# Kernel tuning notes

Measured on AMD Instinct MI355X. Metric: run time of the kernel, lower is better.

Reference implementation:

```python
import jax, jax.numpy as jnp
import numpy as np

N, E, NG = 4096, 8192, 256
AF, BF, H, L = 9, 4, 128, 3
LN_EPS = 1e-5


def _layernorm(x, g, b):
    mu = jnp.mean(x, axis=-1, keepdims=True)
    var = jnp.var(x, axis=-1, keepdims=True)
    return (x - mu) * jax.lax.rsqrt(var + LN_EPS) * g + b


def setup_inputs() -> dict:
    key = jax.random.key(0)
    ks = jax.random.split(key, 20)
    x = jax.random.normal(ks[0], (N, AF), dtype=jnp.float32)
    edge_index = jax.random.randint(ks[1], (2, E), 0, N, dtype=jnp.int64)
    edge_attr = jax.random.normal(ks[2], (E, BF), dtype=jnp.float32)
    batch = jnp.sort(jax.random.randint(ks[3], (N,), 0, NG, dtype=jnp.int64))
    s = lambda f: 1.0 / np.sqrt(f)
    return {
        "x": x, "edge_index": edge_index, "edge_attr": edge_attr, "batch": batch,
        "atom_w": jax.random.normal(ks[4], (AF, H), jnp.float32) * s(AF),
        "atom_b": jnp.zeros((H,), jnp.float32),
        # per-layer edge-network params, stacked over L layers
        "e1_w": jax.random.normal(ks[5], (L, BF, H), jnp.float32) * s(BF),
        "e1_b": jnp.zeros((L, H), jnp.float32),
        "e2_w": jax.random.normal(ks[6], (L, H, H * H), jnp.float32) * s(H),
        "e2_b": jnp.zeros((L, H * H), jnp.float32),
        "root_w": jax.random.normal(ks[7], (L, H, H), jnp.float32) * s(H),
        "conv_b": jnp.zeros((L, H), jnp.float32),
        "ln_g": jnp.ones((L, H), jnp.float32),
        "ln_b": jnp.zeros((L, H), jnp.float32),
        "head_w1": jax.random.normal(ks[8], (H, H // 2), jnp.float32) * s(H),
        "head_b1": jnp.zeros((H // 2,), jnp.float32),
        "head_w2": jax.random.normal(ks[9], (H // 2, 1), jnp.float32) * s(H // 2),
        "head_b2": jnp.zeros((1,), jnp.float32),
    }


def reference(x, edge_index, edge_attr, batch, atom_w, atom_b, e1_w, e1_b,
              e2_w, e2_b, root_w, conv_b, ln_g, ln_b, head_w1, head_b1,
              head_w2, head_b2):
    src, dst = edge_index[0], edge_index[1]
    h = jax.nn.relu(x @ atom_w + atom_b)  # [N, H]
    # in-degree for mean aggregation (empty -> 0 via clamp on denominator)
    deg = jax.ops.segment_sum(jnp.ones((E,), h.dtype), dst, num_segments=N)
    denom = jnp.maximum(deg, 1.0)[:, None]
    for l in range(L):
        # edge network: bond features -> per-edge HxH weight matrix
        eh = jax.nn.gelu(edge_attr @ e1_w[l] + e1_b[l], approximate=False)
        w = (eh @ e2_w[l] + e2_b[l]).reshape(E, H, H)  # [E, H, H]
        # gather source node features, per-edge matvec, scatter-mean to dst
        msg = jnp.einsum('ei,eio->eo', h[src], w)  # [E, H]
        agg = jax.ops.segment_sum(msg, dst, num_segments=N) / denom
        h_new = jax.nn.relu(agg + h @ root_w[l] + conv_b[l])
        h = _layernorm(h + h_new, ln_g[l], ln_b[l])
        # dropout: eval mode (identity)
    # global mean pool over graphs
    cnt = jnp.maximum(jax.ops.segment_sum(jnp.ones((N,), h.dtype), batch, num_segments=NG), 1.0)
    mol = jax.ops.segment_sum(h, batch, num_segments=NG) / cnt[:, None]
    hid = jax.nn.gelu(mol @ head_w1 + head_b1, approximate=False)
    logits = (hid @ head_w2 + head_b2).squeeze(-1)  # [NG]
    return logits
```

## Files before the change

kernel.cpp:

```cpp
#include <hip/hip_runtime.h>
#include <hip/hip_bf16.h>

#define N_NODES 4096
#define N_EDGES 8192
#define NGRAPH  256
#define AFEAT   9
#define BFEAT   4
#define H       128
#define NL      3
#define KS      129
#define SPLITS  4
#define TILE_E  64
#define NPB     4
#define SLICE_SH    16384
#define SLICE_BYTES 32768

typedef short short8 __attribute__((ext_vector_type(8)));
typedef float f32x4 __attribute__((ext_vector_type(4)));

__device__ __forceinline__ short f2b(float f){
    union { float f; unsigned u; } c; c.f = f;
    unsigned r = c.u + 0x7FFFu + ((c.u >> 16) & 1u);
    return (short)(r >> 16);
}
__device__ __forceinline__ float gelu_exact(float x){
    return 0.5f * x * (1.0f + erff(x * 0.70710678118654752440f));
}

__global__ void k_prep_b(const float* __restrict__ e2w, const float* __restrict__ e2b,
                         short* __restrict__ bt){
    __shared__ float ts[H][33];
    int b  = blockIdx.x;
    int o0 = (b & 3) * 32;
    int k  = (b >> 2) % KS;
    int l  = (b >> 2) / KS;
    const float* src = (k < H) ? (e2w + ((size_t)l * H + k) * (H * H))
                               : (e2b + (size_t)l * (H * H));
    for (int idx = threadIdx.x; idx < H * 32; idx += 256){
        int i = idx >> 5, op = idx & 31;
        ts[i][op] = src[i * H + o0 + op];
    }
    __syncthreads();
    short* dst = bt + (size_t)(l * KS + k) * SLICE_SH;
    for (int idx = threadIdx.x; idx < 32 * H; idx += 256){
        int j    = idx & 7;
        int quad = (idx >> 3) & 3;
        int op   = (idx >> 5) & 31;
        int ic   = idx >> 10;
        int i    = ic * 32 + quad * 8 + j;
        int o    = o0 + op;
        dst[((((o >> 4) * 4 + ic) * 64) + quad * 16 + (o & 15)) * 8 + j] = f2b(ts[i][op]);
    }
}

__global__ void k_atom(const float* __restrict__ x, const float* __restrict__ aw,
                       const float* __restrict__ ab, float* __restrict__ h,
                       short* __restrict__ hb){
    __shared__ float xs[AFEAT];
    int n = blockIdx.x, o = threadIdx.x;
    if (o < AFEAT) xs[o] = x[n * AFEAT + o];
    __syncthreads();
    float a = ab[o];
    #pragma unroll
    for (int f = 0; f < AFEAT; ++f) a += xs[f] * aw[f * H + o];
    a = fmaxf(a, 0.0f);
    h[(size_t)n * H + o]  = a;
    hb[(size_t)n * H + o] = f2b(a);
}

__global__ void k_deg(const int* __restrict__ ei, int* __restrict__ ideg){
    int e = blockIdx.x * 256 + threadIdx.x;
    if (e < N_EDGES) atomicAdd(&ideg[ei[N_EDGES + e]], 1);
}

__global__ void k_scan(const int* __restrict__ ideg, int* __restrict__ row_ptr,
                       int* __restrict__ cursor){
    __shared__ int part[256];
    int t = threadIdx.x;
    int base = t * 16;
    int loc[16]; int s = 0;
    #pragma unroll
    for (int i = 0; i < 16; ++i){ loc[i] = s; s += ideg[base + i]; }
    part[t] = s;
    __syncthreads();
    if (t == 0){
        int run = 0;
        for (int i = 0; i < 256; ++i){ int v = part[i]; part[i] = run; run += v; }
        row_ptr[N_NODES] = run;
    }
    __syncthreads();
    int off = part[t];
    #pragma unroll
    for (int i = 0; i < 16; ++i){
        row_ptr[base + i] = off + loc[i];
        cursor[base + i]  = off + loc[i];
    }
}

__global__ void k_fill(const int* __restrict__ ei, int* __restrict__ cursor,
                       int* __restrict__ eidx){
    int e = blockIdx.x * 256 + threadIdx.x;
    if (e < N_EDGES){
        int d = ei[N_EDGES + e];
        int pos = atomicAdd(&cursor[d], 1);
        eidx[pos] = e;
    }
}

__global__ void k_edge_mlp(const float* __restrict__ ea, const float* __restrict__ w1,
                           const float* __restrict__ b1, float* __restrict__ ehT){
    int o = blockIdx.x >> 5;
    int e = (blockIdx.x & 31) * 256 + threadIdx.x;
    float4 a = *(const float4*)(ea + (size_t)e * BFEAT);
    #pragma unroll
    for (int l = 0; l < NL; ++l){
        float v = b1[l * H + o]
                + a.x * w1[(l * BFEAT + 0) * H + o]
                + a.y * w1[(l * BFEAT + 1) * H + o]
                + a.z * w1[(l * BFEAT + 2) * H + o]
                + a.w * w1[(l * BFEAT + 3) * H + o];
        v = gelu_exact(v);
        ehT[((size_t)l * KS + o) * N_EDGES + e] = v;
        if (o == 0) ehT[((size_t)l * KS + H) * N_EDGES + e] = 1.0f;
    }
}

__global__ __launch_bounds__(256, 2)
void k_msg_gemm(const short* __restrict__ bt, const float* __restrict__ ehT,
                const short* __restrict__ hb, const int* __restrict__ ei,
                float* __restrict__ parts, int l){
    __shared__ __align__(16) float ehs[33 * TILE_E];

    const int tid  = threadIdx.x;
    const int lane = tid & 63, w = tid >> 6;
    const int col  = lane & 15, quad = lane >> 4;

    const int so    = blockIdx.x & 7;
    const int split = so & 3;
    const int ohalf = so >> 2;
    const int tile  = blockIdx.x >> 3;
    const int t     = ohalf * 4 + w;
    const int kbeg  = (KS * split) >> 2;
    const int kend  = (KS * (split + 1)) >> 2;
    const int kcnt  = kend - kbeg;
    const int ebase = tile * TILE_E;

    for (int idx = tid; idx < kcnt * TILE_E; idx += 256){
        int kk = idx >> 6, e = idx & 63;
        ehs[idx] = ehT[((size_t)(l * KS + kbeg + kk)) * N_EDGES + ebase + e];
    }

    short8 gf[4][4];
    #pragma unroll
    for (int m = 0; m < 4; ++m){
        int e = ebase + m * 16 + col;
        int s = ei[e];
        const char* gb = (const char*)hb + ((size_t)s * H + quad * 8) * 2;
        #pragma unroll
        for (int ic = 0; ic < 4; ++ic)
            gf[m][ic] = *(const short8*)(gb + ic * 64);
    }

    float acc[4][4];
    #pragma unroll
    for (int m = 0; m < 4; ++m)
        #pragma unroll
        for (int r = 0; r < 4; ++r) acc[m][r] = 0.0f;

    const char* bsrc = (const char*)bt + (size_t)(l * KS + kbeg) * SLICE_BYTES
                     + t * 4096 + lane * 16;

    short8 X[4], Y[4], Z[4];

    auto loadB = [&](short8 (&B)[4], int kk){
        const char* p = bsrc + (size_t)kk * SLICE_BYTES;
        #pragma unroll
        for (int ic = 0; ic < 4; ++ic)
            B[ic] = *(const short8*)(p + ic * 1024);
    };
    auto computeB = [&](const short8 (&B)[4], int kk){
        #pragma unroll
        for (int m = 0; m < 4; ++m){
            f32x4 ev = *(const f32x4*)(ehs + kk * TILE_E + m * 16 + quad * 4);
            f32x4 U = {0.0f, 0.0f, 0.0f, 0.0f};
            #pragma unroll
            for (int ic = 0; ic < 4; ++ic)
                U = __builtin_amdgcn_mfma_f32_16x16x32_bf16(gf[m][ic], B[ic], U, 0, 0, 0);
            #pragma unroll
            for (int r = 0; r < 4; ++r)
                acc[m][r] += ev[r] * U[r];
        }
    };

    loadB(X, 0); loadB(Y, 1); loadB(Z, 2);
    __syncthreads();

    int kk = 0;
    for (; kk + 3 < kcnt; kk += 3){
        computeB(X, kk);     loadB(X, kk + 3);
        computeB(Y, kk + 1); if (kk + 4 < kcnt) loadB(Y, kk + 4);
        computeB(Z, kk + 2); if (kk + 5 < kcnt) loadB(Z, kk + 5);
    }
    computeB(X, kk);
    if (kk + 1 < kcnt) computeB(Y, kk + 1);
    if (kk + 2 < kcnt) computeB(Z, kk + 2);

    float* pb = parts + (size_t)split * N_EDGES * H + (size_t)ebase * H + t * 16;
    #pragma unroll
    for (int m = 0; m < 4; ++m)
        #pragma unroll
        for (int r = 0; r < 4; ++r)
            pb[(size_t)(m * 16 + quad * 4 + r) * H + col] = acc[m][r];
}

__global__ void k_node(const float* __restrict__ parts, const int* __restrict__ eidx,
                       const int* __restrict__ row_ptr,
                       const float* __restrict__ rw, const float* __restrict__ cb,
                       const float* __restrict__ lg, const float* __restrict__ lb,
                       float* __restrict__ h, short* __restrict__ hb,
                       const int* __restrict__ batch, float* __restrict__ molsum,
                       float* __restrict__ cnt, int l, int dolast){
    __shared__ float hs[NPB][H];
    __shared__ float red[NPB][2][2];
    int n0 = blockIdx.x * NPB, o = threadIdx.x;
    const float* W = rw + (size_t)l * H * H;

    float hv[NPB], root[NPB], a[NPB];
    #pragma unroll
    for (int m = 0; m < NPB; ++m){
        hv[m] = h[(size_t)(n0 + m) * H + o];
        hs[m][o] = hv[m];
        root[m] = cb[l * H + o];
    }
    __syncthreads();

    #pragma unroll
    for (int m = 0; m < NPB; ++m){
        int p0 = row_ptr[n0 + m], p1 = row_ptr[n0 + m + 1];
        float s = 0.0f;
        for (int p = p0; p < p1; ++p){
            const float* pr = parts + (size_t)eidx[p] * H + o;
            #pragma unroll
            for (int sp = 0; sp < SPLITS; ++sp) s += pr[(size_t)sp * N_EDGES * H];
        }
        int d = p1 - p0;
        a[m] = s / (float)(d > 0 ? d : 1);
    }

    #pragma unroll 8
    for (int i = 0; i < H; ++i){
        float wv = W[i * H + o];
        #pragma unroll
        for (int m = 0; m < NPB; ++m) root[m] += hs[m][i] * wv;
    }

    float v[NPB];
    #pragma unroll
    for (int m = 0; m < NPB; ++m){
        float hn = fmaxf(a[m] + root[m], 0.0f);
        v[m] = hv[m] + hn;
        float s = v[m], q = v[m] * v[m];
        #pragma unroll
        for (int off = 32; off > 0; off >>= 1){
            s += __shfl_down(s, off, 64);
            q += __shfl_down(q, off, 64);
        }
        if ((o & 63) == 0){ red[m][0][o >> 6] = s; red[m][1][o >> 6] = q; }
    }
    __syncthreads();
    #pragma unroll
    for (int m = 0; m < NPB; ++m){
        float S = red[m][0][0] + red[m][0][1];
        float Q = red[m][1][0] + red[m][1][1];
        float mean = S * (1.0f / H);
        float var  = Q * (1.0f / H) - mean * mean;
        float out  = (v[m] - mean) * rsqrtf(var + 1e-5f) * lg[l * H + o] + lb[l * H + o];
        int n = n0 + m;
        h[(size_t)n * H + o]  = out;
        hb[(size_t)n * H + o] = f2b(out);
        if (dolast){
            int b = batch[n];
            atomicAdd(&molsum[b * H + o], out);
            if (o == 0) atomicAdd(&cnt[b], 1.0f);
        }
    }
}

__global__ void k_head(const float* __restrict__ molsum, const float* __restrict__ cnt,
                       const float* __restrict__ w1, const float* __restrict__ b1,
                       const float* __restrict__ w2, const float* __restrict__ b2,
                       float* __restrict__ out){
    __shared__ float mol[H];
    int g = blockIdx.x, t = threadIdx.x;
    float c = fmaxf(cnt[g], 1.0f);
    mol[t]      = molsum[g * H + t] / c;
    mol[t + 64] = molsum[g * H + t + 64] / c;
    __syncthreads();
    float a = b1[t];
    #pragma unroll 8
    for (int i = 0; i < H; ++i) a += mol[i] * w1[i * 64 + t];
    float hid = gelu_exact(a);
    float p = hid * w2[t];
    #pragma unroll
    for (int off = 32; off > 0; off >>= 1) p += __shfl_down(p, off, 64);
    if (t == 0) out[g] = p + b2[0];
}

extern "C" void kernel_launch(void* const* d_in, const int* in_sizes, int n_in,
                              void* d_out, int out_size, void* d_ws, size_t ws_size,
                              hipStream_t stream){
    (void)in_sizes; (void)n_in; (void)out_size; (void)ws_size;
    const float* x     = (const float*)d_in[0];
    const int*   ei    = (const int*)  d_in[1];
    const float* ea    = (const float*)d_in[2];
    const int*   batch = (const int*)  d_in[3];
    const float* aw    = (const float*)d_in[4];
    const float* ab    = (const float*)d_in[5];
    const float* e1w   = (const float*)d_in[6];
    const float* e1b   = (const float*)d_in[7];
    const float* e2w   = (const float*)d_in[8];
    const float* e2b   = (const float*)d_in[9];
    const float* rw    = (const float*)d_in[10];
    const float* cb    = (const float*)d_in[11];
    const float* lg    = (const float*)d_in[12];
    const float* lb    = (const float*)d_in[13];
    const float* hw1   = (const float*)d_in[14];
    const float* hb1   = (const float*)d_in[15];
    const float* hw2   = (const float*)d_in[16];
    const float* hb2   = (const float*)d_in[17];
    float* out = (float*)d_out;

    char* p = (char*)d_ws;
    auto carve = [&](size_t bytes){ char* r = p; p += (bytes + 255) & ~(size_t)255; return r; };
    short* bt     = (short*)carve((size_t)NL * KS * SLICE_SH * 2);
    float* h      = (float*)carve((size_t)N_NODES * H * 4);
    short* hbuf   = (short*)carve((size_t)N_NODES * H * 2);
    float* ehT    = (float*)carve((size_t)NL * KS * N_EDGES * 4);
    float* parts  = (float*)carve((size_t)SPLITS * N_EDGES * H * 4);
    int*   ideg   = (int*)  carve((size_t)N_NODES * 4);
    int*   row_ptr= (int*)  carve((size_t)(N_NODES + 1) * 4);
    int*   cursor = (int*)  carve((size_t)N_NODES * 4);
    int*   eidx   = (int*)  carve((size_t)N_EDGES * 4);
    float* molsum = (float*)carve((size_t)NGRAPH * H * 4);
    float* cnt    = (float*)carve((size_t)NGRAPH * 4);

    hipMemsetAsync(ideg, 0, (size_t)N_NODES * 4, stream);
    hipMemsetAsync(molsum, 0, (size_t)NGRAPH * H * 4, stream);
    hipMemsetAsync(cnt, 0, (size_t)NGRAPH * 4, stream);

    k_prep_b<<<NL * KS * 4, 256, 0, stream>>>(e2w, e2b, bt);
    k_atom<<<N_NODES, H, 0, stream>>>(x, aw, ab, h, hbuf);
    k_deg<<<N_EDGES / 256, 256, 0, stream>>>(ei, ideg);
    k_scan<<<1, 256, 0, stream>>>(ideg, row_ptr, cursor);
    k_fill<<<N_EDGES / 256, 256, 0, stream>>>(ei, cursor, eidx);
    k_edge_mlp<<<H * (N_EDGES / 256), 256, 0, stream>>>(ea, e1w, e1b, ehT);

    for (int l = 0; l < NL; ++l){
        k_msg_gemm<<<(N_EDGES / TILE_E) * 8, 256, 0, stream>>>(bt, ehT, hbuf, ei, parts, l);
        k_node<<<N_NODES / NPB, H, 0, stream>>>(parts, eidx, row_ptr, rw, cb, lg, lb,
                                                h, hbuf, batch, molsum, cnt, l,
                                                l == NL - 1 ? 1 : 0);
    }
    k_head<<<NGRAPH, 64, 0, stream>>>(molsum, cnt, hw1, hb1, hw2, hb2, out);
}
```

Baseline: 307.6 us.

## Switch message GEMM to 32x32x16 MFMA tiles with two-wave blocks

Rewrites the per-edge message GEMM to use the 32x32x16 bf16 MFMA instruction instead of 16x16x32. The pre-packed edge-weight layout, the source-feature gather, the accumulator shape and the output store are all reorganised to match the new fragment layout. Each block now has 128 threads, with each wave covering 32 output columns. The aim is fewer MFMA issues and less accumulator-scaling overhead per unit of work, at the cost of more registers per wave and fewer waves per block.

```diff
diff --git a/kernel.cpp b/kernel.cpp
--- a/kernel.cpp
+++ b/kernel.cpp
@@ -17,6 +17,7 @@
 
 typedef short short8 __attribute__((ext_vector_type(8)));
 typedef float f32x4 __attribute__((ext_vector_type(4)));
+typedef float f32x16 __attribute__((ext_vector_type(16)));
 
 __device__ __forceinline__ short f2b(float f){
     union { float f; unsigned u; } c; c.f = f;
@@ -42,14 +43,14 @@
     }
     __syncthreads();
     short* dst = bt + (size_t)(l * KS + k) * SLICE_SH;
+    int w32 = o0 >> 5;
     for (int idx = threadIdx.x; idx < 32 * H; idx += 256){
-        int j    = idx & 7;
-        int quad = (idx >> 3) & 3;
-        int op   = (idx >> 5) & 31;
-        int ic   = idx >> 10;
-        int i    = ic * 32 + quad * 8 + j;
-        int o    = o0 + op;
-        dst[((((o >> 4) * 4 + ic) * 64) + quad * 16 + (o & 15)) * 8 + j] = f2b(ts[i][op]);
+        int op = idx & 31;
+        int i  = idx >> 5;
+        int o  = o0 + op;
+        (void)o;
+        dst[(size_t)(w32 * 8 + (i >> 4)) * 512
+            + (op + ((i >> 3) & 1) * 32) * 8 + (i & 7)] = f2b(ts[i][op]);
     }
 }
 
@@ -125,7 +126,7 @@
     }
 }
 
-__global__ __launch_bounds__(256, 2)
+__global__ __launch_bounds__(128, 2)
 void k_msg_gemm(const short* __restrict__ bt, const float* __restrict__ ehT,
                 const short* __restrict__ hb, const int* __restrict__ ei,
                 float* __restrict__ parts, int l){
@@ -133,62 +134,67 @@
 
     const int tid  = threadIdx.x;
     const int lane = tid & 63, w = tid >> 6;
-    const int col  = lane & 15, quad = lane >> 4;
+    const int col  = lane & 31, half = lane >> 5;
 
     const int so    = blockIdx.x & 7;
     const int split = so & 3;
     const int ohalf = so >> 2;
     const int tile  = blockIdx.x >> 3;
-    const int t     = ohalf * 4 + w;
+    const int t32   = ohalf * 2 + w;
     const int kbeg  = (KS * split) >> 2;
     const int kend  = (KS * (split + 1)) >> 2;
     const int kcnt  = kend - kbeg;
     const int ebase = tile * TILE_E;
 
-    for (int idx = tid; idx < kcnt * TILE_E; idx += 256){
+    for (int idx = tid; idx < kcnt * TILE_E; idx += 128){
         int kk = idx >> 6, e = idx & 63;
         ehs[idx] = ehT[((size_t)(l * KS + kbeg + kk)) * N_EDGES + ebase + e];
     }
 
-    short8 gf[4][4];
-    #pragma unroll
-    for (int m = 0; m < 4; ++m){
-        int e = ebase + m * 16 + col;
+    short8 gf[2][8];
+    #pragma unroll
+    for (int m = 0; m < 2; ++m){
+        int e = ebase + m * 32 + col;
         int s = ei[e];
-        const char* gb = (const char*)hb + ((size_t)s * H + quad * 8) * 2;
-        #pragma unroll
-        for (int ic = 0; ic < 4; ++ic)
-            gf[m][ic] = *(const short8*)(gb + ic * 64);
-    }
-
-    float acc[4][4];
-    #pragma unroll
-    for (int m = 0; m < 4; ++m)
-        #pragma unroll
-        for (int r = 0; r < 4; ++r) acc[m][r] = 0.0f;
+        const char* gb = (const char*)hb + ((size_t)s * H + half * 8) * 2;
+        #pragma unroll
+        for (int ic = 0; ic < 8; ++ic)
+            gf[m][ic] = *(const short8*)(gb + ic * 32);
+    }
+
+    f32x16 acc[2];
+    #pragma unroll
+    for (int m = 0; m < 2; ++m)
+        #pragma unroll
+        for (int r = 0; r < 16; ++r) acc[m][r] = 0.0f;
 
     const char* bsrc = (const char*)bt + (size_t)(l * KS + kbeg) * SLICE_BYTES
-                     + t * 4096 + lane * 16;
-
-    short8 X[4], Y[4], Z[4];
-
-    auto loadB = [&](short8 (&B)[4], int kk){
+                     + t32 * 8192 + lane * 16;
+
+    short8 X[8], Y[8], Z[8];
+
+    auto loadB = [&](short8 (&B)[8], int kk){
         const char* p = bsrc + (size_t)kk * SLICE_BYTES;
         #pragma unroll
-        for (int ic = 0; ic < 4; ++ic)
+        for (int ic = 0; ic < 8; ++ic)
             B[ic] = *(const short8*)(p + ic * 1024);
     };
-    auto computeB = [&](const short8 (&B)[4], int kk){
-        #pragma unroll
-        for (int m = 0; m < 4; ++m){
-            f32x4 ev = *(const f32x4*)(ehs + kk * TILE_E + m * 16 + quad * 4);
-            f32x4 U = {0.0f, 0.0f, 0.0f, 0.0f};
-            #pragma unroll
-            for (int ic = 0; ic < 4; ++ic)
-                U = __builtin_amdgcn_mfma_f32_16x16x32_bf16(gf[m][ic], B[ic], U, 0, 0, 0);
-            #pragma unroll
-            for (int r = 0; r < 4; ++r)
-                acc[m][r] += ev[r] * U[r];
+    auto computeB = [&](const short8 (&B)[8], int kk){
+        #pragma unroll
+        for (int m = 0; m < 2; ++m){
+            f32x16 U;
+            #pragma unroll
+            for (int r = 0; r < 16; ++r) U[r] = 0.0f;
+            #pragma unroll
+            for (int ic = 0; ic < 8; ++ic)
+                U = __builtin_amdgcn_mfma_f32_32x32x16_bf16(gf[m][ic], B[ic], U, 0, 0, 0);
+            #pragma unroll
+            for (int q = 0; q < 4; ++q){
+                f32x4 ev = *(const f32x4*)(ehs + kk * TILE_E + m * 32 + q * 8 + half * 4);
+                #pragma unroll
+                for (int r = 0; r < 4; ++r)
+                    acc[m][q * 4 + r] += ev[r] * U[q * 4 + r];
+            }
         }
     };
 
@@ -205,12 +211,14 @@
     if (kk + 1 < kcnt) computeB(Y, kk + 1);
     if (kk + 2 < kcnt) computeB(Z, kk + 2);
 
-    float* pb = parts + (size_t)split * N_EDGES * H + (size_t)ebase * H + t * 16;
-    #pragma unroll
-    for (int m = 0; m < 4; ++m)
-        #pragma unroll
-        for (int r = 0; r < 4; ++r)
-            pb[(size_t)(m * 16 + quad * 4 + r) * H + col] = acc[m][r];
+    float* pb = parts + (size_t)split * N_EDGES * H + (size_t)ebase * H + t32 * 32 + col;
+    #pragma unroll
+    for (int m = 0; m < 2; ++m)
+        #pragma unroll
+        for (int q = 0; q < 4; ++q)
+            #pragma unroll
+            for (int r = 0; r < 4; ++r)
+                pb[(size_t)(m * 32 + q * 8 + half * 4 + r) * H] = acc[m][q * 4 + r];
 }
 
 __global__ void k_node(const float* __restrict__ parts, const int* __restrict__ eidx,
@@ -356,7 +364,7 @@
     k_edge_mlp<<<H * (N_EDGES / 256), 256, 0, stream>>>(ea, e1w, e1b, ehT);
 
     for (int l = 0; l < NL; ++l){
-        k_msg_gemm<<<(N_EDGES / TILE_E) * 8, 256, 0, stream>>>(bt, ehT, hbuf, ei, parts, l);
+        k_msg_gemm<<<(N_EDGES / TILE_E) * 8, 128, 0, stream>>>(bt, ehT, hbuf, ei, parts, l);
         k_node<<<N_NODES / NPB, H, 0, stream>>>(parts, eidx, row_ptr, rw, cb, lg, lb,
                                                 h, hbuf, batch, molsum, cnt, l,
                                                 l == NL - 1 ? 1 : 0);
```

After: 905.9 us. 2.95x slower.

## Stage B slices in LDS via async global-to-LDS copies shared across edge tiles

Applied to the files above, without the earlier changes.

The message GEMM now covers 128 edges per block, split as 2 edge-halves × 2 output subtiles per wave group. Each weight slice is loaded once into a double-buffered LDS staging area with global_load_lds async copies, then shared by both edge halves, instead of every wave loading its B fragments from global memory into registers. The goal is to halve global/L2 traffic for the large per-layer B matrix and overlap the copies with the MFMA work. In exchange it adds two barriers per k-step, more LDS use, and manual vmcnt waits that depend on exact instruction counts.

```diff
diff --git a/kernel.cpp b/kernel.cpp
--- a/kernel.cpp
+++ b/kernel.cpp
@@ -10,7 +10,7 @@
 #define NL      3
 #define KS      129
 #define SPLITS  4
-#define TILE_E  64
+#define TILE_E  128
 #define NPB     4
 #define SLICE_SH    16384
 #define SLICE_BYTES 32768
@@ -25,6 +25,11 @@
 }
 __device__ __forceinline__ float gelu_exact(float x){
     return 0.5f * x * (1.0f + erff(x * 0.70710678118654752440f));
+}
+__device__ __forceinline__ void async_copy16(const void* g, void* l){
+    typedef __attribute__((address_space(1))) const char AS1C;
+    typedef __attribute__((address_space(3))) char AS3;
+    __builtin_amdgcn_global_load_lds((AS1C*)g, (AS3*)l, 16, 0, 0);
 }
 
 __global__ void k_prep_b(const float* __restrict__ e2w, const float* __restrict__ e2b,
@@ -129,31 +134,34 @@
 void k_msg_gemm(const short* __restrict__ bt, const float* __restrict__ ehT,
                 const short* __restrict__ hb, const int* __restrict__ ei,
                 float* __restrict__ parts, int l){
+    __shared__ __align__(16) char bbuf[2][8192];
     __shared__ __align__(16) float ehs[33 * TILE_E];
 
     const int tid  = threadIdx.x;
     const int lane = tid & 63, w = tid >> 6;
     const int col  = lane & 15, quad = lane >> 4;
+    const int we   = w >> 1, wo = w & 1;
 
     const int so    = blockIdx.x & 7;
     const int split = so & 3;
-    const int ohalf = so >> 2;
-    const int tile  = blockIdx.x >> 3;
-    const int t     = ohalf * 4 + w;
+    const int oqh   = so >> 2;
+    const int rest  = blockIdx.x >> 3;
+    const int oq    = oqh * 2 + (rest & 1);
+    const int tile  = rest >> 1;
     const int kbeg  = (KS * split) >> 2;
     const int kend  = (KS * (split + 1)) >> 2;
     const int kcnt  = kend - kbeg;
     const int ebase = tile * TILE_E;
 
     for (int idx = tid; idx < kcnt * TILE_E; idx += 256){
-        int kk = idx >> 6, e = idx & 63;
+        int kk = idx >> 7, e = idx & 127;
         ehs[idx] = ehT[((size_t)(l * KS + kbeg + kk)) * N_EDGES + ebase + e];
     }
 
     short8 gf[4][4];
     #pragma unroll
     for (int m = 0; m < 4; ++m){
-        int e = ebase + m * 16 + col;
+        int e = ebase + we * 64 + m * 16 + col;
         int s = ei[e];
         const char* gb = (const char*)hb + ((size_t)s * H + quad * 8) * 2;
         #pragma unroll
@@ -168,44 +176,47 @@
         for (int r = 0; r < 4; ++r) acc[m][r] = 0.0f;
 
     const char* bsrc = (const char*)bt + (size_t)(l * KS + kbeg) * SLICE_BYTES
-                     + t * 4096 + lane * 16;
-
-    short8 X[4], Y[4], Z[4];
-
-    auto loadB = [&](short8 (&B)[4], int kk){
-        const char* p = bsrc + (size_t)kk * SLICE_BYTES;
+                     + oq * 8192 + w * 2048 + lane * 16;
+
+    async_copy16(bsrc,        bbuf[0] + w * 2048 + lane * 16);
+    async_copy16(bsrc + 1024, bbuf[0] + w * 2048 + 1024 + lane * 16);
+    __syncthreads();
+
+    for (int kk = 0; kk < kcnt; ++kk){
+        __builtin_amdgcn_s_barrier();
+        if (kk + 1 < kcnt){
+            const char* g = bsrc + (size_t)(kk + 1) * SLICE_BYTES;
+            char* d = bbuf[(kk + 1) & 1] + w * 2048 + lane * 16;
+            async_copy16(g,        d);
+            async_copy16(g + 1024, d + 1024);
+            asm volatile("s_waitcnt vmcnt(2)" ::: "memory");
+        } else {
+            asm volatile("s_waitcnt vmcnt(0)" ::: "memory");
+        }
+        __builtin_amdgcn_s_barrier();
+
+        const char* Bl = bbuf[kk & 1] + wo * 4096;
+
+        short8 bf[4];
         #pragma unroll
         for (int ic = 0; ic < 4; ++ic)
-            B[ic] = *(const short8*)(p + ic * 1024);
-    };
-    auto computeB = [&](const short8 (&B)[4], int kk){
+            bf[ic] = *(const short8*)(Bl + ic * 1024 + lane * 16);
+
         #pragma unroll
         for (int m = 0; m < 4; ++m){
-            f32x4 ev = *(const f32x4*)(ehs + kk * TILE_E + m * 16 + quad * 4);
+            f32x4 ev = *(const f32x4*)(ehs + kk * TILE_E + we * 64 + m * 16 + quad * 4);
             f32x4 U = {0.0f, 0.0f, 0.0f, 0.0f};
             #pragma unroll
             for (int ic = 0; ic < 4; ++ic)
-                U = __builtin_amdgcn_mfma_f32_16x16x32_bf16(gf[m][ic], B[ic], U, 0, 0, 0);
+                U = __builtin_amdgcn_mfma_f32_16x16x32_bf16(gf[m][ic], bf[ic], U, 0, 0, 0);
             #pragma unroll
             for (int r = 0; r < 4; ++r)
                 acc[m][r] += ev[r] * U[r];
         }
-    };
-
-    loadB(X, 0); loadB(Y, 1); loadB(Z, 2);
-    __syncthreads();
-
-    int kk = 0;
-    for (; kk + 3 < kcnt; kk += 3){
-        computeB(X, kk);     loadB(X, kk + 3);
-        computeB(Y, kk + 1); if (kk + 4 < kcnt) loadB(Y, kk + 4);
-        computeB(Z, kk + 2); if (kk + 5 < kcnt) loadB(Z, kk + 5);
-    }
-    computeB(X, kk);
-    if (kk + 1 < kcnt) computeB(Y, kk + 1);
-    if (kk + 2 < kcnt) computeB(Z, kk + 2);
-
-    float* pb = parts + (size_t)split * N_EDGES * H + (size_t)ebase * H + t * 16;
+    }
+
+    float* pb = parts + (size_t)split * N_EDGES * H + (size_t)(ebase + we * 64) * H
+              + (oq * 2 + wo) * 16;
     #pragma unroll
     for (int m = 0; m < 4; ++m)
         #pragma unroll
@@ -356,7 +367,7 @@
     k_edge_mlp<<<H * (N_EDGES / 256), 256, 0, stream>>>(ea, e1w, e1b, ehT);
 
     for (int l = 0; l < NL; ++l){
-        k_msg_gemm<<<(N_EDGES / TILE_E) * 8, 256, 0, stream>>>(bt, ehT, hbuf, ei, parts, l);
+        k_msg_gemm<<<(N_EDGES / TILE_E) * 16, 256, 0, stream>>>(bt, ehT, hbuf, ei, parts, l);
         k_node<<<N_NODES / NPB, H, 0, stream>>>(parts, eidx, row_ptr, rw, cb, lg, lb,
                                                 h, hbuf, batch, molsum, cnt, l,
                                                 l == NL - 1 ? 1 : 0);
```

New measurement: 319.6 us. +3.9%, slower.
